# Optimization experiments

Hardware: AMD Instinct MI355X
Metric: run time of the kernel (lower is better)

Reference implementation:

```python
import jax, jax.numpy as jnp
import numpy as np

N_NODES = 50000
N_EDGES = 800000
NFEAT, NHID, NCLASS = 256, 64, 2


def _deg_norm(idx, n_nodes, dtype):
    deg = jax.ops.segment_sum(jnp.ones(idx.shape[0], dtype=dtype), idx, num_segments=n_nodes)
    return jax.lax.rsqrt(jnp.maximum(deg, 1.0))


def gcn_layer(x, W, b, src, dst, n_nodes):
    # DGL GraphConv, norm='both': h = D_in^{-1/2} * Agg( D_out^{-1/2} * x ) W + b
    # weight applied before aggregation (in_feats >= out_feats path); math-equivalent.
    norm_src = _deg_norm(src, n_nodes, x.dtype)  # out-degree norm of source nodes
    norm_dst = _deg_norm(dst, n_nodes, x.dtype)  # in-degree norm of dest nodes
    h = (x * norm_src[:, None]) @ W              # [N, out]
    agg = jax.ops.segment_sum(h[src], dst, num_segments=n_nodes)  # gather + scatter-add
    return agg * norm_dst[:, None] + b


def setup_inputs() -> dict:
    key = jax.random.key(0)
    k1, k2, k3, k4, k5, k6, k7 = jax.random.split(key, 7)
    x = jax.random.normal(k1, (N_NODES, NFEAT), dtype=jnp.float32)
    src = jax.random.randint(k2, (N_EDGES,), 0, N_NODES, dtype=jnp.int64)
    dst = jax.random.randint(k3, (N_EDGES,), 0, N_NODES, dtype=jnp.int64)
    # Glorot-style init like DGL GraphConv
    W1 = jax.random.normal(k4, (NFEAT, NHID), dtype=jnp.float32) * (2.0 / (NFEAT + NHID)) ** 0.5
    b1 = jnp.zeros((NHID,), dtype=jnp.float32)
    W2 = jax.random.normal(k5, (NHID, NCLASS), dtype=jnp.float32) * (2.0 / (NHID + NCLASS)) ** 0.5
    b2 = jnp.zeros((NCLASS,), dtype=jnp.float32)
    return {"x": x, "src": src, "dst": dst, "W1": W1, "b1": b1, "W2": W2, "b2": b2}


def reference(x, src, dst, W1, b1, W2, b2):
    h = jax.nn.relu(gcn_layer(x, W1, b1, src, dst, N_NODES))
    # dropout=False -> p=0, no-op
    logits = gcn_layer(h, W2, b2, src, dst, N_NODES)
    return jax.nn.log_softmax(logits, axis=1)
```

## Files before the change

kernel.cpp:

```cpp
#include <hip/hip_runtime.h>
#include <math.h>

#define N_NODES 50000
#define N_EDGES 800000
#define NFEAT 256
#define NHID 64
#define NCLASS 2

#define NBUCK 196
#define BCAP 8192
#define EPB 2048
#define NB_EDGE ((N_EDGES + EPB - 1) / EPB)

#define OFF_CURD 0
#define OFF_CURS 256
#define OFF_RB   512
#define OFF_DEG  50512
#define OFF_NDST 100512
#define OFF_NSRC 150512
#define OFF_DPK  200512
#define OFF_SV8  1806144
#define OFF_CSR  2207552
#define OFF_HB   3813184
#define OFF_H2   5413184

typedef __attribute__((ext_vector_type(8))) short bf16x8;
typedef __attribute__((ext_vector_type(4))) float f32x4;

static __device__ __forceinline__ unsigned short f2bf(float f) {
    union { float f; unsigned int u; } v; v.f = f;
    unsigned int u = v.u + 0x7fffu + ((v.u >> 16) & 1u);
    return (unsigned short)(u >> 16);
}
static __device__ __forceinline__ float bflo(unsigned int u) {
    union { unsigned int x; float f; } v; v.x = u << 16; return v.f;
}
static __device__ __forceinline__ float bfhi(unsigned int u) {
    union { unsigned int x; float f; } v; v.x = u & 0xffff0000u; return v.f;
}

__global__ __launch_bounds__(256) void bscatter_kernel(const int* __restrict__ src,
                                                       const int* __restrict__ dst,
                                                       int* __restrict__ cur_d,
                                                       int* __restrict__ cur_s,
                                                       int* __restrict__ dpk,
                                                       unsigned char* __restrict__ sv8) {
    __shared__ int hd[256], hs[256], bd[256], bs[256], cd[256], cs[256];
    int t = threadIdx.x;
    hd[t] = 0; hs[t] = 0; cd[t] = 0; cs[t] = 0;
    __syncthreads();
    int base = blockIdx.x * EPB;
    int ls[8], ld[8];
#pragma unroll
    for (int i = 0; i < 8; ++i) {
        int e = base + t + i * 256;
        ls[i] = (e < N_EDGES) ? src[e] : -1;
        ld[i] = (e < N_EDGES) ? dst[e] : -1;
        if (ld[i] >= 0) {
            atomicAdd(&hd[ld[i] >> 8], 1);
            atomicAdd(&hs[ls[i] >> 8], 1);
        }
    }
    __syncthreads();
    if (hd[t]) bd[t] = atomicAdd(&cur_d[t], hd[t]);
    if (hs[t]) bs[t] = atomicAdd(&cur_s[t], hs[t]);
    __syncthreads();
#pragma unroll
    for (int i = 0; i < 8; ++i) {
        if (ld[i] >= 0) {
            int bin = ld[i] >> 8;
            int pos = bd[bin] + atomicAdd(&cd[bin], 1);
            dpk[bin * BCAP + pos] = (ls[i] << 8) | (ld[i] & 255);
            int sbin = ls[i] >> 8;
            int spos = bs[sbin] + atomicAdd(&cs[sbin], 1);
            sv8[sbin * BCAP + spos] = (unsigned char)(ls[i] & 255);
        }
    }
}

__global__ __launch_bounds__(256) void dfin_kernel(const int* __restrict__ cur_d,
                                                   const int* __restrict__ dpk,
                                                   int* __restrict__ row_beg,
                                                   int* __restrict__ degv,
                                                   float* __restrict__ norm_dst,
                                                   int* __restrict__ csr) {
    __shared__ int ebuf[BCAP];
    __shared__ int hist[256], seg[256], cur[256];
    int b = blockIdx.x, t = threadIdx.x;
    int cnt = cur_d[b];
    int base = b * BCAP;
    hist[t] = 0; cur[t] = 0;
    for (int j = t; j < cnt; j += 256) ebuf[j] = dpk[base + j];
    __syncthreads();
    for (int j = t; j < cnt; j += 256) atomicAdd(&hist[ebuf[j] & 255], 1);
    __syncthreads();
    int v = hist[t];
    seg[t] = v;
    __syncthreads();
#pragma unroll
    for (int off = 1; off < 256; off <<= 1) {
        int x = (t >= off) ? seg[t - off] : 0;
        __syncthreads();
        seg[t] += x;
        __syncthreads();
    }
    int excl = seg[t] - v;
    int gid = b * 256 + t;
    if (gid < N_NODES) {
        row_beg[gid] = base + excl;
        degv[gid] = v;
        norm_dst[gid] = rsqrtf(fmaxf((float)v, 1.0f));
    }
    seg[t] = excl;
    __syncthreads();
    for (int j = t; j < cnt; j += 256) {
        int p = ebuf[j];
        int dlow = p & 255;
        int pos = base + seg[dlow] + atomicAdd(&cur[dlow], 1);
        csr[pos] = ((unsigned)p) >> 8;
    }
}

__global__ __launch_bounds__(256) void sfin_kernel(const int* __restrict__ cur_s,
                                                   const unsigned char* __restrict__ sv8,
                                                   float* __restrict__ norm_src) {
    __shared__ int hist[256];
    int b = blockIdx.x, t = threadIdx.x;
    hist[t] = 0;
    __syncthreads();
    int cnt = cur_s[b];
    int base = b * BCAP;
    for (int j = t; j < cnt; j += 256) atomicAdd(&hist[sv8[base + j]], 1);
    __syncthreads();
    int gid = b * 256 + t;
    if (gid < N_NODES) norm_src[gid] = rsqrtf(fmaxf((float)hist[t], 1.0f));
}

#define LDA 264
__global__ __launch_bounds__(256) void gemm1_kernel(const float* __restrict__ x,
                                                    const float* __restrict__ W1,
                                                    const float* __restrict__ norm_src,
                                                    unsigned short* __restrict__ hb) {
    __shared__ unsigned short As[64][LDA];
    __shared__ unsigned short Bs[64][LDA];
    const int t = threadIdx.x;
    const int row0 = blockIdx.x * 64;
#pragma unroll
    for (int i = 0; i < 16; ++i) {
        int f = i * 256 + t;
        int r = f >> 6;
        int c4 = (f & 63) * 4;
        int grow = row0 + r;
        float4 av = make_float4(0.f, 0.f, 0.f, 0.f);
        float nrm = 0.f;
        if (grow < N_NODES) {
            av = *(const float4*)(&x[(size_t)grow * NFEAT + c4]);
            nrm = norm_src[grow];
        }
        ushort4 o;
        o.x = f2bf(av.x * nrm); o.y = f2bf(av.y * nrm);
        o.z = f2bf(av.z * nrm); o.w = f2bf(av.w * nrm);
        *(ushort4*)(&As[r][c4]) = o;
    }
#pragma unroll
    for (int i = 0; i < 16; ++i) {
        int f = i * 256 + t;
        int k = f >> 4;
        int n4 = (f & 15) * 4;
        float4 wv = *(const float4*)(&W1[k * NHID + n4]);
        Bs[n4 + 0][k] = f2bf(wv.x);
        Bs[n4 + 1][k] = f2bf(wv.y);
        Bs[n4 + 2][k] = f2bf(wv.z);
        Bs[n4 + 3][k] = f2bf(wv.w);
    }
    __syncthreads();
    const int w = t >> 6;
    const int l = t & 63;
    const int m = l & 15;
    const int kq = (l >> 4) * 8;
    f32x4 acc[4] = {{0.f, 0.f, 0.f, 0.f}, {0.f, 0.f, 0.f, 0.f},
                    {0.f, 0.f, 0.f, 0.f}, {0.f, 0.f, 0.f, 0.f}};
#pragma unroll
    for (int c8 = 0; c8 < 8; ++c8) {
        int k0 = c8 * 32 + kq;
        bf16x8 a = *(const bf16x8*)(&As[w * 16 + m][k0]);
#pragma unroll
        for (int ct = 0; ct < 4; ++ct) {
            bf16x8 b = *(const bf16x8*)(&Bs[ct * 16 + m][k0]);
            acc[ct] = __builtin_amdgcn_mfma_f32_16x16x32_bf16(a, b, acc[ct], 0, 0, 0);
        }
    }
    const int q = l >> 4;
#pragma unroll
    for (int ct = 0; ct < 4; ++ct) {
#pragma unroll
        for (int reg = 0; reg < 4; ++reg) {
            int r = row0 + w * 16 + q * 4 + reg;
            if (r < N_NODES) hb[(size_t)r * NHID + ct * 16 + m] = f2bf(acc[ct][reg]);
        }
    }
}

__global__ __launch_bounds__(256) void fused1_kernel(const int* __restrict__ row_beg,
                                                     const int* __restrict__ degv,
                                                     const int* __restrict__ csr,
                                                     const unsigned short* __restrict__ hb,
                                                     const float* __restrict__ norm_dst,
                                                     const float* __restrict__ norm_src,
                                                     const float* __restrict__ b1,
                                                     const float* __restrict__ W2,
                                                     float* __restrict__ h2) {
    int gtid = blockIdx.x * blockDim.x + threadIdx.x;
    int node = gtid >> 6;
    int lane = gtid & 63;
    if (node >= N_NODES) return;
    int e8 = lane >> 3, fg = lane & 7;
    int beg = row_beg[node];
    int end = beg + degv[node];
    float a0 = 0.f, a1 = 0.f, a2 = 0.f, a3 = 0.f, a4 = 0.f, a5 = 0.f, a6 = 0.f, a7 = 0.f;
    for (int j = beg; j < end; j += 16) {
        int j0 = j + e8, j1 = j0 + 8;
        uint4 u0 = make_uint4(0u, 0u, 0u, 0u), u1 = make_uint4(0u, 0u, 0u, 0u);
        if (j0 < end) u0 = *(const uint4*)(&hb[(size_t)csr[j0] * NHID + fg * 8]);
        if (j1 < end) u1 = *(const uint4*)(&hb[(size_t)csr[j1] * NHID + fg * 8]);
        a0 += bflo(u0.x) + bflo(u1.x);
        a1 += bfhi(u0.x) + bfhi(u1.x);
        a2 += bflo(u0.y) + bflo(u1.y);
        a3 += bfhi(u0.y) + bfhi(u1.y);
        a4 += bflo(u0.z) + bflo(u1.z);
        a5 += bfhi(u0.z) + bfhi(u1.z);
        a6 += bflo(u0.w) + bflo(u1.w);
        a7 += bfhi(u0.w) + bfhi(u1.w);
    }
#pragma unroll
    for (int off = 8; off <= 32; off <<= 1) {
        a0 += __shfl_xor(a0, off, 64);
        a1 += __shfl_xor(a1, off, 64);
        a2 += __shfl_xor(a2, off, 64);
        a3 += __shfl_xor(a3, off, 64);
        a4 += __shfl_xor(a4, off, 64);
        a5 += __shfl_xor(a5, off, 64);
        a6 += __shfl_xor(a6, off, 64);
        a7 += __shfl_xor(a7, off, 64);
    }
    float nd = norm_dst[node], ns = norm_src[node];
    float4 bv0 = *(const float4*)(&b1[fg * 8]);
    float4 bv1 = *(const float4*)(&b1[fg * 8 + 4]);
    float4 w0 = *(const float4*)(&W2[fg * 16 + 0]);
    float4 w1 = *(const float4*)(&W2[fg * 16 + 4]);
    float4 w2v = *(const float4*)(&W2[fg * 16 + 8]);
    float4 w3 = *(const float4*)(&W2[fg * 16 + 12]);
    float h0 = fmaxf(fmaf(a0, nd, bv0.x), 0.f) * ns;
    float h1 = fmaxf(fmaf(a1, nd, bv0.y), 0.f) * ns;
    float h2f = fmaxf(fmaf(a2, nd, bv0.z), 0.f) * ns;
    float h3 = fmaxf(fmaf(a3, nd, bv0.w), 0.f) * ns;
    float h4 = fmaxf(fmaf(a4, nd, bv1.x), 0.f) * ns;
    float h5 = fmaxf(fmaf(a5, nd, bv1.y), 0.f) * ns;
    float h6 = fmaxf(fmaf(a6, nd, bv1.z), 0.f) * ns;
    float h7 = fmaxf(fmaf(a7, nd, bv1.w), 0.f) * ns;
    float p0 = h0 * w0.x + h1 * w0.z + h2f * w1.x + h3 * w1.z +
               h4 * w2v.x + h5 * w2v.z + h6 * w3.x + h7 * w3.z;
    float p1 = h0 * w0.y + h1 * w0.w + h2f * w1.y + h3 * w1.w +
               h4 * w2v.y + h5 * w2v.w + h6 * w3.y + h7 * w3.w;
#pragma unroll
    for (int off = 1; off <= 4; off <<= 1) {
        p0 += __shfl_xor(p0, off, 64);
        p1 += __shfl_xor(p1, off, 64);
    }
    if (lane == 0) *(float2*)(&h2[node * 2]) = make_float2(p0, p1);
}

__global__ void fused2_kernel(const int* __restrict__ row_beg, const int* __restrict__ degv,
                              const int* __restrict__ csr, const float* __restrict__ h2,
                              const float* __restrict__ norm_dst, const float* __restrict__ b2,
                              float* __restrict__ out) {
    int n = blockIdx.x * blockDim.x + threadIdx.x;
    if (n >= N_NODES) return;
    int beg = row_beg[n], end = beg + degv[n];
    float s0 = 0.f, s1 = 0.f;
    for (int j = beg; j < end; ++j) {
        float2 v = *(const float2*)(&h2[csr[j] * 2]);
        s0 += v.x;
        s1 += v.y;
    }
    float nd = norm_dst[n];
    float l0 = fmaf(s0, nd, b2[0]);
    float l1 = fmaf(s1, nd, b2[1]);
    float m = fmaxf(l0, l1);
    float lse = m + logf(expf(l0 - m) + expf(l1 - m));
    *(float2*)(&out[n * 2]) = make_float2(l0 - lse, l1 - lse);
}

extern "C" void kernel_launch(void* const* d_in, const int* in_sizes, int n_in,
                              void* d_out, int out_size, void* d_ws, size_t ws_size,
                              hipStream_t stream) {
    const float* x  = (const float*)d_in[0];
    const int* src  = (const int*)d_in[1];
    const int* dst  = (const int*)d_in[2];
    const float* W1 = (const float*)d_in[3];
    const float* b1 = (const float*)d_in[4];
    const float* W2 = (const float*)d_in[5];
    const float* b2 = (const float*)d_in[6];
    float* out = (float*)d_out;
    float* ws  = (float*)d_ws;
    int*   wsi = (int*)d_ws;

    int*   cur_d    = wsi + OFF_CURD;
    int*   cur_s    = wsi + OFF_CURS;
    int*   row_beg  = wsi + OFF_RB;
    int*   degv     = wsi + OFF_DEG;
    float* norm_dst = ws + OFF_NDST;
    float* norm_src = ws + OFF_NSRC;
    int*   dpk      = wsi + OFF_DPK;
    unsigned char* sv8 = (unsigned char*)(wsi + OFF_SV8);
    int*   csr      = wsi + OFF_CSR;
    unsigned short* hb = (unsigned short*)(wsi + OFF_HB);
    float* h2       = ws + OFF_H2;

    hipMemsetAsync(cur_d, 0, 512 * sizeof(int), stream);
    bscatter_kernel<<<NB_EDGE, 256, 0, stream>>>(src, dst, cur_d, cur_s, dpk, sv8);
    dfin_kernel<<<NBUCK, 256, 0, stream>>>(cur_d, dpk, row_beg, degv, norm_dst, csr);
    sfin_kernel<<<NBUCK, 256, 0, stream>>>(cur_s, sv8, norm_src);
    gemm1_kernel<<<(N_NODES + 63) / 64, 256, 0, stream>>>(x, W1, norm_src, hb);
    {
        long long threads = (long long)N_NODES * 64;
        fused1_kernel<<<(int)((threads + 255) / 256), 256, 0, stream>>>(
            row_beg, degv, csr, hb, norm_dst, norm_src, b1, W2, h2);
    }
    fused2_kernel<<<(N_NODES + 255) / 256, 256, 0, stream>>>(row_beg, degv, csr, h2, norm_dst, b2, out);
}
```

Before: 189.5 us.

## Use finer 64-node buckets, pre-transposed bf16 W1, and epilogue norm scaling

Node buckets shrink from 256 to 64 nodes, raising the number of dfin/sfin blocks from 196 to 782 and making the histograms four-way privatized to cut LDS atomic contention. W1 is converted to a transposed bf16 copy by a separate small kernel, so gemm1 loads it with vector loads instead of each block converting and transposing it. The norm_src scaling moves from the input rows to the GEMM epilogue, and bf16 packing uses a perm-based round-half-up instead of round-to-nearest-even. This adds one kernel launch and a larger bscatter shared-memory footprint, and changes bf16 rounding slightly.

```diff
diff --git a/kernel.cpp b/kernel.cpp
--- a/kernel.cpp
+++ b/kernel.cpp
@@ -7,36 +7,51 @@
 #define NHID 64
 #define NCLASS 2
 
-#define NBUCK 196
-#define BCAP 8192
+#define DB 64
+#define NDB 782
+#define BCAP 1536
 #define EPB 2048
 #define NB_EDGE ((N_EDGES + EPB - 1) / EPB)
 
 #define OFF_CURD 0
-#define OFF_CURS 256
-#define OFF_RB   512
-#define OFF_DEG  50512
-#define OFF_NDST 100512
-#define OFF_NSRC 150512
-#define OFF_DPK  200512
-#define OFF_SV8  1806144
-#define OFF_CSR  2207552
-#define OFF_HB   3813184
-#define OFF_H2   5413184
+#define OFF_CURS 800
+#define OFF_RB   1600
+#define OFF_DEG  51600
+#define OFF_NDST 101600
+#define OFF_NSRC 151600
+#define OFF_W1T  201600
+#define OFF_DPK  209792
+#define OFF_SV6  1410944
+#define OFF_CSR  1711232
+#define OFF_HB   2912384
+#define OFF_H2   4512384
 
 typedef __attribute__((ext_vector_type(8))) short bf16x8;
+typedef __attribute__((ext_vector_type(8))) short short8;
 typedef __attribute__((ext_vector_type(4))) float f32x4;
 
 static __device__ __forceinline__ unsigned short f2bf(float f) {
     union { float f; unsigned int u; } v; v.f = f;
-    unsigned int u = v.u + 0x7fffu + ((v.u >> 16) & 1u);
-    return (unsigned short)(u >> 16);
+    return (unsigned short)((v.u + 0x8000u) >> 16);
+}
+static __device__ __forceinline__ unsigned int pk2bf(float f0, float f1) {
+    union { float f; unsigned int u; } a, b; a.f = f0; b.f = f1;
+    return __builtin_amdgcn_perm(b.u + 0x8000u, a.u + 0x8000u, 0x07060302u);
 }
 static __device__ __forceinline__ float bflo(unsigned int u) {
     union { unsigned int x; float f; } v; v.x = u << 16; return v.f;
 }
 static __device__ __forceinline__ float bfhi(unsigned int u) {
     union { unsigned int x; float f; } v; v.x = u & 0xffff0000u; return v.f;
+}
+
+__global__ __launch_bounds__(256) void w1cvt_kernel(const float* __restrict__ W1,
+                                                    unsigned short* __restrict__ w1t) {
+    int idx = blockIdx.x * 256 + threadIdx.x;
+    if (idx < NFEAT * NHID) {
+        int k = idx >> 6, n = idx & 63;
+        w1t[n * NFEAT + k] = f2bf(W1[idx]);
+    }
 }
 
 __global__ __launch_bounds__(256) void bscatter_kernel(const int* __restrict__ src,
@@ -44,10 +59,10 @@
                                                        int* __restrict__ cur_d,
                                                        int* __restrict__ cur_s,
                                                        int* __restrict__ dpk,
-                                                       unsigned char* __restrict__ sv8) {
-    __shared__ int hd[256], hs[256], bd[256], bs[256], cd[256], cs[256];
+                                                       unsigned char* __restrict__ sv6) {
+    __shared__ int hd[NDB], bd[NDB], cd[NDB], hs[NDB], bs[NDB], cs[NDB];
     int t = threadIdx.x;
-    hd[t] = 0; hs[t] = 0; cd[t] = 0; cs[t] = 0;
+    for (int i = t; i < NDB; i += 256) { hd[i] = 0; cd[i] = 0; hs[i] = 0; cs[i] = 0; }
     __syncthreads();
     int base = blockIdx.x * EPB;
     int ls[8], ld[8];
@@ -57,23 +72,25 @@
         ls[i] = (e < N_EDGES) ? src[e] : -1;
         ld[i] = (e < N_EDGES) ? dst[e] : -1;
         if (ld[i] >= 0) {
-            atomicAdd(&hd[ld[i] >> 8], 1);
-            atomicAdd(&hs[ls[i] >> 8], 1);
-        }
-    }
-    __syncthreads();
-    if (hd[t]) bd[t] = atomicAdd(&cur_d[t], hd[t]);
-    if (hs[t]) bs[t] = atomicAdd(&cur_s[t], hs[t]);
+            atomicAdd(&hd[ld[i] >> 6], 1);
+            atomicAdd(&hs[ls[i] >> 6], 1);
+        }
+    }
+    __syncthreads();
+    for (int i = t; i < NDB; i += 256) {
+        if (hd[i]) bd[i] = atomicAdd(&cur_d[i], hd[i]);
+        if (hs[i]) bs[i] = atomicAdd(&cur_s[i], hs[i]);
+    }
     __syncthreads();
 #pragma unroll
     for (int i = 0; i < 8; ++i) {
         if (ld[i] >= 0) {
-            int bin = ld[i] >> 8;
+            int bin = ld[i] >> 6;
             int pos = bd[bin] + atomicAdd(&cd[bin], 1);
-            dpk[bin * BCAP + pos] = (ls[i] << 8) | (ld[i] & 255);
-            int sbin = ls[i] >> 8;
+            dpk[bin * BCAP + pos] = (ls[i] << 6) | (ld[i] & 63);
+            int sbin = ls[i] >> 6;
             int spos = bs[sbin] + atomicAdd(&cs[sbin], 1);
-            sv8[sbin * BCAP + spos] = (unsigned char)(ls[i] & 255);
+            sv6[sbin * BCAP + spos] = (unsigned char)(ls[i] & 63);
         }
     }
 }
@@ -85,60 +102,75 @@
                                                    float* __restrict__ norm_dst,
                                                    int* __restrict__ csr) {
     __shared__ int ebuf[BCAP];
-    __shared__ int hist[256], seg[256], cur[256];
+    __shared__ int hist4[4 * 64], hist[64], seg[64], cur[64];
     int b = blockIdx.x, t = threadIdx.x;
     int cnt = cur_d[b];
     int base = b * BCAP;
-    hist[t] = 0; cur[t] = 0;
+    if (t < 64) { hist[t] = 0; cur[t] = 0; }
+    hist4[t] = 0;
     for (int j = t; j < cnt; j += 256) ebuf[j] = dpk[base + j];
     __syncthreads();
-    for (int j = t; j < cnt; j += 256) atomicAdd(&hist[ebuf[j] & 255], 1);
-    __syncthreads();
-    int v = hist[t];
-    seg[t] = v;
-    __syncthreads();
-#pragma unroll
-    for (int off = 1; off < 256; off <<= 1) {
-        int x = (t >= off) ? seg[t - off] : 0;
+    int sub = (t & 3) * 64;
+    for (int j = t; j < cnt; j += 256) atomicAdd(&hist4[sub + (ebuf[j] & 63)], 1);
+    __syncthreads();
+    if (t < 64) {
+        int v = hist4[t] + hist4[64 + t] + hist4[128 + t] + hist4[192 + t];
+        hist[t] = v;
+        seg[t] = v;
+    }
+    __syncthreads();
+#pragma unroll
+    for (int off = 1; off < 64; off <<= 1) {
+        int xv = 0;
+        if (t < 64 && t >= off) xv = seg[t - off];
         __syncthreads();
-        seg[t] += x;
+        if (t < 64) seg[t] += xv;
         __syncthreads();
     }
-    int excl = seg[t] - v;
-    int gid = b * 256 + t;
-    if (gid < N_NODES) {
-        row_beg[gid] = base + excl;
-        degv[gid] = v;
-        norm_dst[gid] = rsqrtf(fmaxf((float)v, 1.0f));
-    }
-    seg[t] = excl;
+    if (t < 64) {
+        int v = hist[t];
+        int excl = seg[t] - v;
+        int gid = b * 64 + t;
+        if (gid < N_NODES) {
+            row_beg[gid] = base + excl;
+            degv[gid] = v;
+            norm_dst[gid] = rsqrtf(fmaxf((float)v, 1.0f));
+        }
+        seg[t] = excl;
+    }
     __syncthreads();
     for (int j = t; j < cnt; j += 256) {
         int p = ebuf[j];
-        int dlow = p & 255;
+        int dlow = p & 63;
         int pos = base + seg[dlow] + atomicAdd(&cur[dlow], 1);
-        csr[pos] = ((unsigned)p) >> 8;
+        csr[pos] = ((unsigned)p) >> 6;
     }
 }
 
 __global__ __launch_bounds__(256) void sfin_kernel(const int* __restrict__ cur_s,
-                                                   const unsigned char* __restrict__ sv8,
+                                                   const unsigned char* __restrict__ sv6,
                                                    float* __restrict__ norm_src) {
-    __shared__ int hist[256];
+    __shared__ int hist4[4 * 64];
     int b = blockIdx.x, t = threadIdx.x;
-    hist[t] = 0;
+    hist4[t] = 0;
     __syncthreads();
     int cnt = cur_s[b];
     int base = b * BCAP;
-    for (int j = t; j < cnt; j += 256) atomicAdd(&hist[sv8[base + j]], 1);
-    __syncthreads();
-    int gid = b * 256 + t;
-    if (gid < N_NODES) norm_src[gid] = rsqrtf(fmaxf((float)hist[t], 1.0f));
+    int sub = (t & 3) * 64;
+    for (int j = t; j < cnt; j += 256) atomicAdd(&hist4[sub + sv6[base + j]], 1);
+    __syncthreads();
+    if (t < 64) {
+        int gid = b * 64 + t;
+        if (gid < N_NODES) {
+            int v = hist4[t] + hist4[64 + t] + hist4[128 + t] + hist4[192 + t];
+            norm_src[gid] = rsqrtf(fmaxf((float)v, 1.0f));
+        }
+    }
 }
 
 #define LDA 264
 __global__ __launch_bounds__(256) void gemm1_kernel(const float* __restrict__ x,
-                                                    const float* __restrict__ W1,
+                                                    const unsigned short* __restrict__ w1t,
                                                     const float* __restrict__ norm_src,
                                                     unsigned short* __restrict__ hb) {
     __shared__ unsigned short As[64][LDA];
@@ -152,26 +184,18 @@
         int c4 = (f & 63) * 4;
         int grow = row0 + r;
         float4 av = make_float4(0.f, 0.f, 0.f, 0.f);
-        float nrm = 0.f;
-        if (grow < N_NODES) {
-            av = *(const float4*)(&x[(size_t)grow * NFEAT + c4]);
-            nrm = norm_src[grow];
-        }
-        ushort4 o;
-        o.x = f2bf(av.x * nrm); o.y = f2bf(av.y * nrm);
-        o.z = f2bf(av.z * nrm); o.w = f2bf(av.w * nrm);
-        *(ushort4*)(&As[r][c4]) = o;
-    }
-#pragma unroll
-    for (int i = 0; i < 16; ++i) {
-        int f = i * 256 + t;
-        int k = f >> 4;
-        int n4 = (f & 15) * 4;
-        float4 wv = *(const float4*)(&W1[k * NHID + n4]);
-        Bs[n4 + 0][k] = f2bf(wv.x);
-        Bs[n4 + 1][k] = f2bf(wv.y);
-        Bs[n4 + 2][k] = f2bf(wv.z);
-        Bs[n4 + 3][k] = f2bf(wv.w);
+        if (grow < N_NODES) av = *(const float4*)(&x[(size_t)grow * NFEAT + c4]);
+        uint2 o;
+        o.x = pk2bf(av.x, av.y);
+        o.y = pk2bf(av.z, av.w);
+        *(uint2*)(&As[r][c4]) = o;
+    }
+#pragma unroll
+    for (int i = 0; i < 8; ++i) {
+        int c = i * 256 + t;
+        int n = c >> 5;
+        int k8 = (c & 31) * 8;
+        *(short8*)(&Bs[n][k8]) = *(const short8*)(&w1t[n * NFEAT + k8]);
     }
     __syncthreads();
     const int w = t >> 6;
@@ -192,11 +216,13 @@
     }
     const int q = l >> 4;
 #pragma unroll
-    for (int ct = 0; ct < 4; ++ct) {
-#pragma unroll
-        for (int reg = 0; reg < 4; ++reg) {
-            int r = row0 + w * 16 + q * 4 + reg;
-            if (r < N_NODES) hb[(size_t)r * NHID + ct * 16 + m] = f2bf(acc[ct][reg]);
+    for (int reg = 0; reg < 4; ++reg) {
+        int r = row0 + w * 16 + q * 4 + reg;
+        if (r < N_NODES) {
+            float ns = norm_src[r];
+#pragma unroll
+            for (int ct = 0; ct < 4; ++ct)
+                hb[(size_t)r * NHID + ct * 16 + m] = f2bf(acc[ct][reg] * ns);
         }
     }
 }
@@ -311,17 +337,19 @@
     int*   degv     = wsi + OFF_DEG;
     float* norm_dst = ws + OFF_NDST;
     float* norm_src = ws + OFF_NSRC;
+    unsigned short* w1t = (unsigned short*)(wsi + OFF_W1T);
     int*   dpk      = wsi + OFF_DPK;
-    unsigned char* sv8 = (unsigned char*)(wsi + OFF_SV8);
+    unsigned char* sv6 = (unsigned char*)(wsi + OFF_SV6);
     int*   csr      = wsi + OFF_CSR;
     unsigned short* hb = (unsigned short*)(wsi + OFF_HB);
     float* h2       = ws + OFF_H2;
 
-    hipMemsetAsync(cur_d, 0, 512 * sizeof(int), stream);
-    bscatter_kernel<<<NB_EDGE, 256, 0, stream>>>(src, dst, cur_d, cur_s, dpk, sv8);
-    dfin_kernel<<<NBUCK, 256, 0, stream>>>(cur_d, dpk, row_beg, degv, norm_dst, csr);
-    sfin_kernel<<<NBUCK, 256, 0, stream>>>(cur_s, sv8, norm_src);
-    gemm1_kernel<<<(N_NODES + 63) / 64, 256, 0, stream>>>(x, W1, norm_src, hb);
+    hipMemsetAsync(cur_d, 0, 1600 * sizeof(int), stream);
+    w1cvt_kernel<<<(NFEAT * NHID + 255) / 256, 256, 0, stream>>>(W1, w1t);
+    bscatter_kernel<<<NB_EDGE, 256, 0, stream>>>(src, dst, cur_d, cur_s, dpk, sv6);
+    sfin_kernel<<<NDB, 256, 0, stream>>>(cur_s, sv6, norm_src);
+    dfin_kernel<<<NDB, 256, 0, stream>>>(cur_d, dpk, row_beg, degv, norm_dst, csr);
+    gemm1_kernel<<<(N_NODES + 63) / 64, 256, 0, stream>>>(x, w1t, norm_src, hb);
     {
         long long threads = (long long)N_NODES * 64;
         fused1_kernel<<<(int)((threads + 255) / 256), 256, 0, stream>>>(
```

Result: no change. 191.1 us (+0.9%).
